# Performance work log

Hardware: AMD Instinct MI355X
Metric: run time of the kernel (lower is better)

The kernel has to match this reference:

```python
import jax, jax.numpy as jnp
import numpy as np

N = 50000      # nodes
E = 800000     # edges
P = 200000     # link pairs
D_IN = 128     # input_dim
F_NUM = 128    # filter_num
OUT = 2        # out_dim
K = 10         # APPNP propagation steps
ALPHA = 0.1    # teleport prob


def setup_inputs() -> dict:
    key = jax.random.key(0)
    ks = jax.random.split(key, 9)
    x = jax.random.normal(ks[0], (N, D_IN), dtype=jnp.float32)
    edge_index = jax.random.randint(ks[1], (2, E), 0, N)
    index = jax.random.randint(ks[2], (P, 2), 0, N)
    s1 = 1.0 / np.sqrt(D_IN)
    s2 = 1.0 / np.sqrt(F_NUM)
    s3 = 1.0 / np.sqrt(2 * F_NUM)
    W1 = jax.random.uniform(ks[3], (F_NUM, D_IN), minval=-s1, maxval=s1)
    b1 = jax.random.uniform(ks[4], (F_NUM,), minval=-s1, maxval=s1)
    W2 = jax.random.uniform(ks[5], (F_NUM, F_NUM), minval=-s2, maxval=s2)
    b2 = jax.random.uniform(ks[6], (F_NUM,), minval=-s2, maxval=s2)
    W3 = jax.random.uniform(ks[7], (OUT, 2 * F_NUM), minval=-s3, maxval=s3)
    b3 = jax.random.uniform(ks[8], (OUT,), minval=-s3, maxval=s3)
    return {"x": x, "edge_index": edge_index, "index": index,
            "W1": W1, "b1": b1, "W2": W2, "b2": b2, "W3": W3, "b3": b3}


def _gcn_norm(edge_index, num_nodes):
    # PyG gcn_norm: add self-loops, sym norm D^{-1/2} (A+I) D^{-1/2}
    src, dst = edge_index[0], edge_index[1]
    loop = jnp.arange(num_nodes, dtype=src.dtype)
    src = jnp.concatenate([src, loop])
    dst = jnp.concatenate([dst, loop])
    deg = jax.ops.segment_sum(jnp.ones_like(src, dtype=jnp.float32), dst,
                              num_segments=num_nodes)
    dinv = jnp.where(deg > 0, jax.lax.rsqrt(deg), 0.0)
    norm = dinv[src] * dinv[dst]  # [E+N]
    return src, dst, norm


def _appnp(x, src, dst, norm, num_nodes):
    # h_{k+1} = (1-alpha) * A_hat h_k + alpha * x0
    def step(h, _):
        agg = jax.ops.segment_sum(norm[:, None] * h[src], dst,
                                  num_segments=num_nodes)
        return (1.0 - ALPHA) * agg + ALPHA * x, None
    h, _ = jax.lax.scan(step, x, None, length=K)
    return h


def reference(x, edge_index, index, W1, b1, W2, b2, W3, b3):
    num_nodes = x.shape[0]
    src, dst, norm = _gcn_norm(edge_index, num_nodes)
    h = x @ W1.T + b1                      # [N, F]
    h = jax.nn.relu(_appnp(h, src, dst, norm, num_nodes))
    h = h @ W2.T + b2                      # [N, F]
    h = jax.nn.relu(_appnp(h, src, dst, norm, num_nodes))
    feat = jnp.concatenate([h[index[:, 0]], h[index[:, 1]]], axis=-1)  # [P, 2F]
    out = feat @ W3.T + b3                 # [P, OUT]
    return jax.nn.log_softmax(out, axis=1)
```

## Files before the change

kernel.cpp:

```cpp
#include <hip/hip_runtime.h>
#include <math.h>

#define NN 50000
#define NE 800000
#define NP 200000
#define NF 128
#define NEDGE_TOT (NE + NN)
#define NBLK 196

typedef __attribute__((ext_vector_type(8))) short short8;
typedef __attribute__((ext_vector_type(4))) float float4v;

__device__ __forceinline__ float bf_lo(unsigned u) { return __uint_as_float(u << 16); }
__device__ __forceinline__ float bf_hi(unsigned u) { return __uint_as_float(u & 0xffff0000u); }
__device__ __forceinline__ unsigned short f2bf(float f) {
    unsigned u = __float_as_uint(f);
    return (unsigned short)((u + 0x7fffu + ((u >> 16) & 1u)) >> 16);
}
__device__ __forceinline__ unsigned pack2bf(float a, float b) {
    return (unsigned)f2bf(a) | ((unsigned)f2bf(b) << 16);
}

__global__ __launch_bounds__(256) void init_cnt_k(int* __restrict__ cnt) {
    int i = blockIdx.x * 256 + threadIdx.x;
    if (i < NN) cnt[i] = 1;
}

__global__ __launch_bounds__(256) void count_k(const int* __restrict__ ei,
                                               int* __restrict__ cnt) {
    int e = blockIdx.x * 256 + threadIdx.x;
    if (e < NE) atomicAdd(&cnt[ei[NE + e]], 1);
}

__global__ __launch_bounds__(256) void scan_reduce_k(const int* __restrict__ cnt,
                                                     int* __restrict__ bsum,
                                                     float* __restrict__ dinv) {
    __shared__ int s[256];
    int t = threadIdx.x;
    int idx = blockIdx.x * 256 + t;
    int v = (idx < NN) ? cnt[idx] : 0;
    if (idx < NN) dinv[idx] = rsqrtf((float)v);
    s[t] = v;
    __syncthreads();
    for (int off = 128; off > 0; off >>= 1) {
        if (t < off) s[t] += s[t + off];
        __syncthreads();
    }
    if (t == 0) bsum[blockIdx.x] = s[0];
}

__global__ __launch_bounds__(256) void scan_bsums_k(const int* __restrict__ bsum,
                                                    int* __restrict__ boff) {
    __shared__ int s[256];
    int t = threadIdx.x;
    int v = (t < NBLK) ? bsum[t] : 0;
    s[t] = v;
    __syncthreads();
    for (int off = 1; off < 256; off <<= 1) {
        int add = (t >= off) ? s[t - off] : 0;
        __syncthreads();
        s[t] += add;
        __syncthreads();
    }
    if (t < NBLK) boff[t] = s[t] - v;
}

__global__ __launch_bounds__(256) void scan_down_k(const int* __restrict__ cnt,
                                                   const int* __restrict__ boff,
                                                   int* __restrict__ row_ptr,
                                                   int* __restrict__ wptr) {
    __shared__ int s[256];
    int t = threadIdx.x;
    int idx = blockIdx.x * 256 + t;
    int v = (idx < NN) ? cnt[idx] : 0;
    s[t] = v;
    __syncthreads();
    for (int off = 1; off < 256; off <<= 1) {
        int add = (t >= off) ? s[t - off] : 0;
        __syncthreads();
        s[t] += add;
        __syncthreads();
    }
    int excl = s[t] - v + boff[blockIdx.x];
    if (idx < NN) {
        row_ptr[idx] = excl;
        wptr[idx] = excl;
        if (idx == NN - 1) row_ptr[NN] = excl + v;
    }
}

__global__ __launch_bounds__(256) void scatter_k(const int* __restrict__ ei,
                                                 int* __restrict__ wptr,
                                                 int* __restrict__ cols) {
    int e = blockIdx.x * 256 + threadIdx.x;
    if (e >= NEDGE_TOT) return;
    int s, d;
    if (e < NE) { s = ei[e]; d = ei[NE + e]; }
    else        { s = d = e - NE; }
    int pos = atomicAdd(&wptr[d], 1);
    cols[pos] = s;
}

__global__ __launch_bounds__(256) void zero_k(unsigned short* Ys1, unsigned short* Ys2,
                                              unsigned short* HA, unsigned short* HB) {
    int t = threadIdx.x;
    unsigned short* bufs[4] = {Ys1, Ys2, HA, HB};
    unsigned short* b = bufs[t >> 6];
    ((unsigned*)(b + (size_t)NN * NF))[t & 63] = 0u;
}

__global__ __launch_bounds__(256) void cast_w_k(const float* __restrict__ W,
                                                unsigned short* __restrict__ Wb) {
    int t = blockIdx.x * 256 + threadIdx.x;
    if (t >= 128 * 128 / 8) return;
    int i = t * 8;
    float4 f0 = *(const float4*)(W + i);
    float4 f1 = *(const float4*)(W + i + 4);
    uint4 q;
    q.x = pack2bf(f0.x, f0.y);
    q.y = pack2bf(f0.z, f0.w);
    q.z = pack2bf(f1.x, f1.y);
    q.w = pack2bf(f1.z, f1.w);
    *(uint4*)(Wb + i) = q;
}

#define GPAD 136
template <bool F32IN>
__global__ __launch_bounds__(256) void gemm_mfma_k(const void* __restrict__ Xv,
                                                   const unsigned short* __restrict__ Wb,
                                                   const float* __restrict__ bias,
                                                   const float* __restrict__ dinv,
                                                   unsigned short* __restrict__ Yu,
                                                   unsigned short* __restrict__ Ys,
                                                   int nrows) {
    __shared__ unsigned short sm[4 * 16 * GPAD];
    int wave = threadIdx.x >> 6, lane = threadIdx.x & 63;
    int rbase = blockIdx.x * 64 + wave * 16;
    if (rbase >= nrows) return;
    int quad = lane >> 4, mn = lane & 15;
    float4v acc[8];
#pragma unroll
    for (int ft = 0; ft < 8; ++ft) acc[ft] = (float4v){0.f, 0.f, 0.f, 0.f};
#pragma unroll
    for (int kb = 0; kb < 128; kb += 32) {
        short8 a;
        if (F32IN) {
            const float* X = (const float*)Xv;
            float4 f0 = *(const float4*)(X + (size_t)(rbase + mn) * NF + kb + quad * 8);
            float4 f1 = *(const float4*)(X + (size_t)(rbase + mn) * NF + kb + quad * 8 + 4);
            a[0] = (short)f2bf(f0.x); a[1] = (short)f2bf(f0.y);
            a[2] = (short)f2bf(f0.z); a[3] = (short)f2bf(f0.w);
            a[4] = (short)f2bf(f1.x); a[5] = (short)f2bf(f1.y);
            a[6] = (short)f2bf(f1.z); a[7] = (short)f2bf(f1.w);
        } else {
            const unsigned short* X = (const unsigned short*)Xv;
            a = *(const short8*)(X + (size_t)(rbase + mn) * NF + kb + quad * 8);
        }
#pragma unroll
        for (int ft = 0; ft < 8; ++ft) {
            short8 b = *(const short8*)(Wb + (size_t)(ft * 16 + mn) * NF + kb + quad * 8);
            acc[ft] = __builtin_amdgcn_mfma_f32_16x16x32_bf16(a, b, acc[ft], 0, 0, 0);
        }
    }
    unsigned short* smw = sm + wave * 16 * GPAD;
#pragma unroll
    for (int ft = 0; ft < 8; ++ft) {
        float bv = bias[ft * 16 + mn];
#pragma unroll
        for (int r = 0; r < 4; ++r)
            smw[(quad * 4 + r) * GPAD + ft * 16 + mn] = f2bf(acc[ft][r] + bv);
    }
    __syncthreads();
#pragma unroll
    for (int t = 0; t < 4; ++t) {
        int rl = t * 4 + quad;
        int row = rbase + rl;
        uint4 q = *(const uint4*)(smw + rl * GPAD + mn * 8);
        *(uint4*)(Yu + (size_t)row * NF + mn * 8) = q;
        float g = dinv[row];
        uint4 qs;
        qs.x = pack2bf(g * bf_lo(q.x), g * bf_hi(q.x));
        qs.y = pack2bf(g * bf_lo(q.y), g * bf_hi(q.y));
        qs.z = pack2bf(g * bf_lo(q.z), g * bf_hi(q.z));
        qs.w = pack2bf(g * bf_lo(q.w), g * bf_hi(q.w));
        *(uint4*)(Ys + (size_t)row * NF + mn * 8) = qs;
    }
}

__global__ __launch_bounds__(256) void appnp_s_k(const unsigned short* __restrict__ hs,
                                                 const unsigned short* __restrict__ x0,
                                                 const float* __restrict__ dinv,
                                                 unsigned short* __restrict__ out,
                                                 const int* __restrict__ row_ptr,
                                                 const int* __restrict__ cols,
                                                 int mode,
                                                 const float* __restrict__ W3,
                                                 float4* __restrict__ puv) {
    int wid = (blockIdx.x * 256 + threadIdx.x) >> 6;
    int lane = threadIdx.x & 63;
    if (wid >= NN) return;
    int half = lane >> 5, li = lane & 31;
    int beg = row_ptr[wid], end = row_ptr[wid + 1];
    float a0 = 0.f, a1 = 0.f, a2 = 0.f, a3 = 0.f;
    for (int e = beg; e < end; e += 64) {
        int m = end - e;
        if (m > 64) m = 64;
        int c = (lane < m) ? cols[e + lane] : NN;
        int j = 0;
        for (; j + 8 <= m; j += 8) {
            int c0 = __shfl(c, j + half, 64);
            int c1 = __shfl(c, j + 2 + half, 64);
            int c2 = __shfl(c, j + 4 + half, 64);
            int c3 = __shfl(c, j + 6 + half, 64);
            uint2 q0 = *((const uint2*)(hs + (size_t)c0 * NF) + li);
            uint2 q1 = *((const uint2*)(hs + (size_t)c1 * NF) + li);
            uint2 q2 = *((const uint2*)(hs + (size_t)c2 * NF) + li);
            uint2 q3 = *((const uint2*)(hs + (size_t)c3 * NF) + li);
            a0 += (bf_lo(q0.x) + bf_lo(q1.x)) + (bf_lo(q2.x) + bf_lo(q3.x));
            a1 += (bf_hi(q0.x) + bf_hi(q1.x)) + (bf_hi(q2.x) + bf_hi(q3.x));
            a2 += (bf_lo(q0.y) + bf_lo(q1.y)) + (bf_lo(q2.y) + bf_lo(q3.y));
            a3 += (bf_hi(q0.y) + bf_hi(q1.y)) + (bf_hi(q2.y) + bf_hi(q3.y));
        }
        for (; j < m; j += 2) {
            int cj = __shfl(c, j + half, 64);
            uint2 q = *((const uint2*)(hs + (size_t)cj * NF) + li);
            a0 += bf_lo(q.x);
            a1 += bf_hi(q.x);
            a2 += bf_lo(q.y);
            a3 += bf_hi(q.y);
        }
    }
    a0 += __shfl_xor(a0, 32, 64);
    a1 += __shfl_xor(a1, 32, 64);
    a2 += __shfl_xor(a2, 32, 64);
    a3 += __shfl_xor(a3, 32, 64);
    if (half == 0) {
        float g = dinv[wid];
        float s9 = 0.9f * g;
        uint2 xq = *((const uint2*)(x0 + (size_t)wid * NF) + li);
        float h0 = s9 * a0 + 0.1f * bf_lo(xq.x);
        float h1 = s9 * a1 + 0.1f * bf_hi(xq.x);
        float h2 = s9 * a2 + 0.1f * bf_lo(xq.y);
        float h3 = s9 * a3 + 0.1f * bf_hi(xq.y);
        if (mode == 0) {
            uint2 oq;
            oq.x = pack2bf(g * h0, g * h1);
            oq.y = pack2bf(g * h2, g * h3);
            *((uint2*)(out + (size_t)wid * NF) + li) = oq;
        } else {
            h0 = fmaxf(h0, 0.f); h1 = fmaxf(h1, 0.f);
            h2 = fmaxf(h2, 0.f); h3 = fmaxf(h3, 0.f);
            if (mode == 1) {
                uint2 oq;
                oq.x = pack2bf(h0, h1);
                oq.y = pack2bf(h2, h3);
                *((uint2*)(out + (size_t)wid * NF) + li) = oq;
            } else {
                int fb = li * 4;
                float4 wu0 = *(const float4*)(W3 + fb);
                float4 wv0 = *(const float4*)(W3 + 128 + fb);
                float4 wu1 = *(const float4*)(W3 + 256 + fb);
                float4 wv1 = *(const float4*)(W3 + 384 + fb);
                float du0 = h0 * wu0.x + h1 * wu0.y + h2 * wu0.z + h3 * wu0.w;
                float du1 = h0 * wu1.x + h1 * wu1.y + h2 * wu1.z + h3 * wu1.w;
                float dv0 = h0 * wv0.x + h1 * wv0.y + h2 * wv0.z + h3 * wv0.w;
                float dv1 = h0 * wv1.x + h1 * wv1.y + h2 * wv1.z + h3 * wv1.w;
#pragma unroll
                for (int off = 1; off < 32; off <<= 1) {
                    du0 += __shfl_xor(du0, off, 64);
                    du1 += __shfl_xor(du1, off, 64);
                    dv0 += __shfl_xor(dv0, off, 64);
                    dv1 += __shfl_xor(dv1, off, 64);
                }
                if (li == 0) puv[wid] = make_float4(du0, du1, dv0, dv1);
            }
        }
    }
}

__global__ __launch_bounds__(256) void pair2_k(const float4* __restrict__ puv,
                                               const int2* __restrict__ index,
                                               const float* __restrict__ b3,
                                               float* __restrict__ outp) {
    int p = blockIdx.x * 256 + threadIdx.x;
    if (p >= NP) return;
    int2 uv = index[p];
    float4 a = puv[uv.x];
    float4 b = puv[uv.y];
    float s0 = a.x + b.z + b3[0];
    float s1 = a.y + b.w + b3[1];
    float m = fmaxf(s0, s1);
    float lse = m + logf(expf(s0 - m) + expf(s1 - m));
    *(float2*)(outp + (size_t)p * 2) = make_float2(s0 - lse, s1 - lse);
}

extern "C" void kernel_launch(void* const* d_in, const int* in_sizes, int n_in,
                              void* d_out, int out_size, void* d_ws, size_t ws_size,
                              hipStream_t stream) {
    const float* x  = (const float*)d_in[0];
    const int* ei   = (const int*)d_in[1];
    const int* idx  = (const int*)d_in[2];
    const float* W1 = (const float*)d_in[3];
    const float* b1 = (const float*)d_in[4];
    const float* W2 = (const float*)d_in[5];
    const float* b2 = (const float*)d_in[6];
    const float* W3 = (const float*)d_in[7];
    const float* b3 = (const float*)d_in[8];
    float* out = (float*)d_out;

    char* ws = (char*)d_ws;
    size_t off = 0;
    auto alloc = [&](size_t bytes) -> void* {
        void* p = ws + off;
        off = (off + bytes + 255) & ~(size_t)255;
        return p;
    };
    const size_t HROWS = (size_t)(NN + 1) * NF;
    int*   cnt     = (int*)  alloc(NN * sizeof(int));
    float* dinv    = (float*)alloc(NN * sizeof(float));
    int*   row_ptr = (int*)  alloc((NN + 1) * sizeof(int));
    int*   wptr    = (int*)  alloc(NN * sizeof(int));
    int*   bsum    = (int*)  alloc(NBLK * sizeof(int));
    int*   boff    = (int*)  alloc(NBLK * sizeof(int));
    int*   cols    = (int*)  alloc((size_t)NEDGE_TOT * sizeof(int));
    float4* puv    = (float4*)alloc((size_t)NN * sizeof(float4));
    unsigned short* Wb1 = (unsigned short*)alloc(128 * 128 * 2);
    unsigned short* Wb2 = (unsigned short*)alloc(128 * 128 * 2);
    unsigned short* Yu1 = (unsigned short*)alloc(HROWS * 2);
    unsigned short* Ys1 = (unsigned short*)alloc(HROWS * 2);
    unsigned short* Yu2 = (unsigned short*)alloc(HROWS * 2);
    unsigned short* Ys2 = (unsigned short*)alloc(HROWS * 2);
    unsigned short* HA  = (unsigned short*)alloc(HROWS * 2);
    unsigned short* HB  = (unsigned short*)alloc(HROWS * 2);
    unsigned short* Hrelu = (unsigned short*)alloc((size_t)NN * NF * 2);

    const int gN    = (NN + 255) / 256;
    const int gE    = (NE + 255) / 256;
    const int gET   = (NEDGE_TOT + 255) / 256;
    const int gGemm = (NN + 63) / 64;
    const int gStep = (NN * 64 + 255) / 256;
    const int gPair = (NP + 255) / 256;

    cast_w_k<<<8, 256, 0, stream>>>(W1, Wb1);
    cast_w_k<<<8, 256, 0, stream>>>(W2, Wb2);
    init_cnt_k<<<gN, 256, 0, stream>>>(cnt);
    count_k<<<gE, 256, 0, stream>>>(ei, cnt);
    scan_reduce_k<<<NBLK, 256, 0, stream>>>(cnt, bsum, dinv);
    scan_bsums_k<<<1, 256, 0, stream>>>(bsum, boff);
    scan_down_k<<<NBLK, 256, 0, stream>>>(cnt, boff, row_ptr, wptr);
    scatter_k<<<gET, 256, 0, stream>>>(ei, wptr, cols);
    zero_k<<<1, 256, 0, stream>>>(Ys1, Ys2, HA, HB);

    gemm_mfma_k<true><<<gGemm, 256, 0, stream>>>(x, Wb1, b1, dinv, Yu1, Ys1, NN);
    {
        const unsigned short* cur = Ys1;
        for (int k = 0; k < 10; ++k) {
            unsigned short* dst = (k == 9) ? Hrelu : ((k & 1) ? HB : HA);
            appnp_s_k<<<gStep, 256, 0, stream>>>(cur, Yu1, dinv, dst, row_ptr,
                                                 cols, (k == 9) ? 1 : 0, W3, puv);
            cur = dst;
        }
    }
    gemm_mfma_k<false><<<gGemm, 256, 0, stream>>>(Hrelu, Wb2, b2, dinv, Yu2, Ys2, NN);
    {
        const unsigned short* cur = Ys2;
        for (int k = 0; k < 10; ++k) {
            unsigned short* dst = (k & 1) ? HB : HA;
            appnp_s_k<<<gStep, 256, 0, stream>>>(cur, Yu2, dinv, dst, row_ptr,
                                                 cols, (k == 9) ? 2 : 0, W3, puv);
            cur = dst;
        }
    }
    pair2_k<<<gPair, 256, 0, stream>>>(puv, (const int2*)idx, b3, out);
}
```

Baseline: 883.3 us.

## Build CSR via two-pass bucketed binning instead of global atomic scatter

Replaces the global-atomic edge scatter with a two-stage build. First, edges are binned by destination range into 64 buckets, using shared-memory staging and one global atomic per bucket per block. Then one block per bucket places columns using LDS atomics on its local write pointers. The aim is to cut contended global atomics and scattered writes during CSR construction, at the cost of an extra intermediate buffer with a fixed per-bucket capacity, which could overflow on skewed degree distributions. The APPNP gather inner loop is also simplified to a single 8-edge unrolled loop that relies on padded column entries, removing the remainder loop.

```diff
diff --git a/kernel.cpp b/kernel.cpp
--- a/kernel.cpp
+++ b/kernel.cpp
@@ -7,6 +7,10 @@
 #define NF 128
 #define NEDGE_TOT (NE + NN)
 #define NBLK 196
+#define NBK 64
+#define DPB 782
+#define BKCAP 16384
+#define EPB 2048
 
 typedef __attribute__((ext_vector_type(8))) short short8;
 typedef __attribute__((ext_vector_type(4))) float float4v;
@@ -67,8 +71,7 @@
 
 __global__ __launch_bounds__(256) void scan_down_k(const int* __restrict__ cnt,
                                                    const int* __restrict__ boff,
-                                                   int* __restrict__ row_ptr,
-                                                   int* __restrict__ wptr) {
+                                                   int* __restrict__ row_ptr) {
     __shared__ int s[256];
     int t = threadIdx.x;
     int idx = blockIdx.x * 256 + t;
@@ -84,29 +87,88 @@
     int excl = s[t] - v + boff[blockIdx.x];
     if (idx < NN) {
         row_ptr[idx] = excl;
-        wptr[idx] = excl;
         if (idx == NN - 1) row_ptr[NN] = excl + v;
     }
 }
 
-__global__ __launch_bounds__(256) void scatter_k(const int* __restrict__ ei,
-                                                 int* __restrict__ wptr,
-                                                 int* __restrict__ cols) {
-    int e = blockIdx.x * 256 + threadIdx.x;
-    if (e >= NEDGE_TOT) return;
-    int s, d;
-    if (e < NE) { s = ei[e]; d = ei[NE + e]; }
-    else        { s = d = e - NE; }
-    int pos = atomicAdd(&wptr[d], 1);
-    cols[pos] = s;
+__global__ __launch_bounds__(256) void bin_k(const int* __restrict__ ei,
+                                             int* __restrict__ gtail,
+                                             int2* __restrict__ gbk) {
+    __shared__ int cntA[NBK], baseA[NBK], gposA[NBK];
+    __shared__ int2 stage[EPB];
+    int tid = threadIdx.x;
+    int ebase = blockIdx.x * EPB;
+    int sv[8], dv[8], lp8[8], bk8[8];
+    bool val[8];
+    if (tid < NBK) cntA[tid] = 0;
+    __syncthreads();
+#pragma unroll
+    for (int k = 0; k < 8; ++k) {
+        int e = ebase + k * 256 + tid;
+        val[k] = (e < NEDGE_TOT);
+        if (val[k]) {
+            int s, d;
+            if (e < NE) { s = ei[e]; d = ei[NE + e]; }
+            else        { s = d = e - NE; }
+            sv[k] = s; dv[k] = d;
+            bk8[k] = d / DPB;
+            lp8[k] = atomicAdd(&cntA[bk8[k]], 1);
+        }
+    }
+    __syncthreads();
+    if (tid == 0) {
+        int run = 0;
+        for (int b = 0; b < NBK; ++b) { baseA[b] = run; run += cntA[b]; }
+    }
+    __syncthreads();
+    if (tid < NBK && cntA[tid] > 0)
+        gposA[tid] = atomicAdd(&gtail[tid], cntA[tid]);
+    __syncthreads();
+#pragma unroll
+    for (int k = 0; k < 8; ++k)
+        if (val[k]) {
+            int2 r; r.x = sv[k]; r.y = dv[k];
+            stage[baseA[bk8[k]] + lp8[k]] = r;
+        }
+    __syncthreads();
+    int total = baseA[NBK - 1] + cntA[NBK - 1];
+    for (int i = tid; i < total; i += 256) {
+        int2 r = stage[i];
+        int b = r.y / DPB;
+        gbk[(size_t)b * BKCAP + gposA[b] + (i - baseA[b])] = r;
+    }
+}
+
+__global__ __launch_bounds__(256) void build_k(const int* __restrict__ row_ptr,
+                                               const int* __restrict__ gtail,
+                                               const int2* __restrict__ gbk,
+                                               int* __restrict__ cols) {
+    __shared__ int wcur[DPB];
+    int tid = threadIdx.x;
+    int b = blockIdx.x;
+    int d0 = b * DPB;
+    for (int i = tid; i < DPB; i += 256) {
+        int d = d0 + i;
+        wcur[i] = (d < NN) ? row_ptr[d] : 0;
+    }
+    __syncthreads();
+    int nb = gtail[b];
+    const int2* src = gbk + (size_t)b * BKCAP;
+    for (int t = tid; t < nb; t += 256) {
+        int2 r = src[t];
+        int pos = atomicAdd(&wcur[r.y - d0], 1);
+        cols[pos] = r.x;
+    }
 }
 
 __global__ __launch_bounds__(256) void zero_k(unsigned short* Ys1, unsigned short* Ys2,
-                                              unsigned short* HA, unsigned short* HB) {
+                                              unsigned short* HA, unsigned short* HB,
+                                              int* gtail) {
     int t = threadIdx.x;
     unsigned short* bufs[4] = {Ys1, Ys2, HA, HB};
     unsigned short* b = bufs[t >> 6];
     ((unsigned*)(b + (size_t)NN * NF))[t & 63] = 0u;
+    if (t < NBK) gtail[t] = 0;
 }
 
 __global__ __launch_bounds__(256) void cast_w_k(const float* __restrict__ W,
@@ -206,28 +268,16 @@
         int m = end - e;
         if (m > 64) m = 64;
         int c = (lane < m) ? cols[e + lane] : NN;
-        int j = 0;
-        for (; j + 8 <= m; j += 8) {
-            int c0 = __shfl(c, j + half, 64);
-            int c1 = __shfl(c, j + 2 + half, 64);
-            int c2 = __shfl(c, j + 4 + half, 64);
-            int c3 = __shfl(c, j + 6 + half, 64);
-            uint2 q0 = *((const uint2*)(hs + (size_t)c0 * NF) + li);
-            uint2 q1 = *((const uint2*)(hs + (size_t)c1 * NF) + li);
-            uint2 q2 = *((const uint2*)(hs + (size_t)c2 * NF) + li);
-            uint2 q3 = *((const uint2*)(hs + (size_t)c3 * NF) + li);
-            a0 += (bf_lo(q0.x) + bf_lo(q1.x)) + (bf_lo(q2.x) + bf_lo(q3.x));
-            a1 += (bf_hi(q0.x) + bf_hi(q1.x)) + (bf_hi(q2.x) + bf_hi(q3.x));
-            a2 += (bf_lo(q0.y) + bf_lo(q1.y)) + (bf_lo(q2.y) + bf_lo(q3.y));
-            a3 += (bf_hi(q0.y) + bf_hi(q1.y)) + (bf_hi(q2.y) + bf_hi(q3.y));
-        }
-        for (; j < m; j += 2) {
-            int cj = __shfl(c, j + half, 64);
-            uint2 q = *((const uint2*)(hs + (size_t)cj * NF) + li);
-            a0 += bf_lo(q.x);
-            a1 += bf_hi(q.x);
-            a2 += bf_lo(q.y);
-            a3 += bf_hi(q.y);
+        for (int j = 0; j < m; j += 8) {
+#pragma unroll
+            for (int p = 0; p < 4; ++p) {
+                int cj = __shfl(c, j + 2 * p + half, 64);
+                uint2 q = *((const uint2*)(hs + (size_t)cj * NF) + li);
+                a0 += bf_lo(q.x);
+                a1 += bf_hi(q.x);
+                a2 += bf_lo(q.y);
+                a3 += bf_hi(q.y);
+            }
         }
     }
     a0 += __shfl_xor(a0, 32, 64);
@@ -319,9 +369,10 @@
     int*   cnt     = (int*)  alloc(NN * sizeof(int));
     float* dinv    = (float*)alloc(NN * sizeof(float));
     int*   row_ptr = (int*)  alloc((NN + 1) * sizeof(int));
-    int*   wptr    = (int*)  alloc(NN * sizeof(int));
     int*   bsum    = (int*)  alloc(NBLK * sizeof(int));
     int*   boff    = (int*)  alloc(NBLK * sizeof(int));
+    int*   gtail   = (int*)  alloc(NBK * sizeof(int));
+    int2*  gbk     = (int2*) alloc((size_t)NBK * BKCAP * sizeof(int2));
     int*   cols    = (int*)  alloc((size_t)NEDGE_TOT * sizeof(int));
     float4* puv    = (float4*)alloc((size_t)NN * sizeof(float4));
     unsigned short* Wb1 = (unsigned short*)alloc(128 * 128 * 2);
@@ -336,20 +387,21 @@
 
     const int gN    = (NN + 255) / 256;
     const int gE    = (NE + 255) / 256;
-    const int gET   = (NEDGE_TOT + 255) / 256;
+    const int gBin  = (NEDGE_TOT + EPB - 1) / EPB;
     const int gGemm = (NN + 63) / 64;
     const int gStep = (NN * 64 + 255) / 256;
     const int gPair = (NP + 255) / 256;
 
     cast_w_k<<<8, 256, 0, stream>>>(W1, Wb1);
     cast_w_k<<<8, 256, 0, stream>>>(W2, Wb2);
+    zero_k<<<1, 256, 0, stream>>>(Ys1, Ys2, HA, HB, gtail);
     init_cnt_k<<<gN, 256, 0, stream>>>(cnt);
     count_k<<<gE, 256, 0, stream>>>(ei, cnt);
     scan_reduce_k<<<NBLK, 256, 0, stream>>>(cnt, bsum, dinv);
     scan_bsums_k<<<1, 256, 0, stream>>>(bsum, boff);
-    scan_down_k<<<NBLK, 256, 0, stream>>>(cnt, boff, row_ptr, wptr);
-    scatter_k<<<gET, 256, 0, stream>>>(ei, wptr, cols);
-    zero_k<<<1, 256, 0, stream>>>(Ys1, Ys2, HA, HB);
+    scan_down_k<<<NBLK, 256, 0, stream>>>(cnt, boff, row_ptr);
+    bin_k<<<gBin, 256, 0, stream>>>(ei, gtail, gbk);
+    build_k<<<NBK, 256, 0, stream>>>(row_ptr, gtail, gbk, cols);
 
     gemm_mfma_k<true><<<gGemm, 256, 0, stream>>>(x, Wb1, b1, dinv, Yu1, Ys1, NN);
     {
```

Measured after the change: 832.3 us. -5.8%, faster.
